# Kernel optimization log

Measured on AMD Instinct MI355X. Metric: run time of the kernel, lower is better.

The kernel has to match this reference:

```python
import jax, jax.numpy as jnp
import numpy as np

CHAR_DIM = 96
COLOR_DIM = 16
GLYPH_DIM = CHAR_DIM * COLOR_DIM  # 1536 bounded id space
CHAR_EMB = 16
COLOR_EMB = 4
GLYPH_EMB = CHAR_EMB + COLOR_EMB  # 20
HID = 32
MAX_LEN = 64


def setup_inputs() -> dict:
    key = jax.random.key(0)
    ks = jax.random.split(key, 8)
    B, H, W = 4096, 21, 79
    glyph_chars = jax.random.randint(ks[0], (B, H, W), 0, CHAR_DIM)
    glyph_colors = jax.random.randint(ks[1], (B, H, W), 0, COLOR_DIM)
    # embedding tables (row CHAR_DIM / COLOR_DIM is the padding row)
    char_table = jax.random.normal(ks[2], (CHAR_DIM + 1, CHAR_EMB), jnp.float32) * 0.1
    col_table = jax.random.normal(ks[3], (COLOR_DIM + 1, COLOR_EMB), jnp.float32) * 0.1
    s = 1.0 / np.sqrt(HID)
    Wih = jax.random.uniform(ks[4], (HID, GLYPH_EMB), jnp.float32, -s, s)
    Whh = jax.random.uniform(ks[5], (HID, HID), jnp.float32, -s, s)
    bih = jax.random.uniform(ks[6], (HID,), jnp.float32, -s, s)
    bhh = jax.random.uniform(ks[7], (HID,), jnp.float32, -s, s)
    return dict(glyph_chars=glyph_chars, glyph_colors=glyph_colors,
                char_table=char_table, col_table=col_table,
                Wih=Wih, Whh=Whh, bih=bih, bhh=bhh)


def reference(glyph_chars, glyph_colors, char_table, col_table, Wih, Whh, bih, bhh):
    B = glyph_chars.shape[0]
    # combined glyph id in the bounded [0, GLYPH_DIM) space
    ids = (glyph_chars * COLOR_DIM + glyph_colors).reshape(B, -1)  # [B, H*W]
    # batched fixed-size histogram over the bounded id space (replaces per-sample torch.unique)
    counts = jnp.zeros((B, GLYPH_DIM), jnp.int32).at[jnp.arange(B)[:, None], ids].add(1)
    present = counts > 0  # [B, GLYPH_DIM]
    # sorted unique ids (ascending == lexicographic over (char,color)); absent ids pushed to GLYPH_DIM
    sorted_ids = jnp.sort(jnp.where(present, jnp.arange(GLYPH_DIM), GLYPH_DIM), axis=-1)[:, :MAX_LEN]
    is_pad = sorted_ids >= GLYPH_DIM
    char_bag = jnp.where(is_pad, CHAR_DIM, sorted_ids // COLOR_DIM)   # pad -> CHAR_DIM row
    color_bag = jnp.where(is_pad, COLOR_DIM, sorted_ids % COLOR_DIM)  # pad -> COLOR_DIM row
    bag = jnp.stack([char_bag, color_bag], axis=-1)  # [B, MAX_LEN, 2]
    lengths = jnp.minimum(present.sum(-1), MAX_LEN)  # [B]
    emb = jnp.concatenate([char_table[char_bag], col_table[color_bag]], axis=-1)  # [B, MAX_LEN, 20]
    # vanilla tanh RNN over the packed (variable-length) bag; keep hidden at last valid step
    def step(h, inp):
        x_t, t = inp  # x_t: [B, 20]
        h_new = jnp.tanh(x_t @ Wih.T + bih + h @ Whh.T + bhh)
        h = jnp.where((t < lengths)[:, None], h_new, h)
        return h, None
    h0 = jnp.zeros((B, HID), emb.dtype)
    h, _ = jax.lax.scan(step, h0, (emb.transpose(1, 0, 2), jnp.arange(MAX_LEN)))
    return h, emb, bag
```

## Files before the change

kernel.cpp:

```cpp
#include <hip/hip_runtime.h>
#include <hip/hip_bf16.h>

#define HW        1659
#define GLYPH_DIM 1536
#define NBL       16
#define THREADS   1024

typedef _Float16 half8  __attribute__((ext_vector_type(8)));
typedef _Float16 half2v __attribute__((ext_vector_type(2)));
typedef float    f32x4  __attribute__((ext_vector_type(4)));

__device__ __forceinline__ float tanh_f(float x) {
    float e = __expf(x + x);
    return fmaf(-2.0f, __builtin_amdgcn_rcpf(e + 1.0f), 1.0f);
}

__device__ __forceinline__ unsigned int pk(float a, float b) {
    return __builtin_bit_cast(unsigned int, __builtin_amdgcn_cvt_pkrtz(a, b));
}

__device__ __forceinline__ half8 h8(unsigned int a, unsigned int b,
                                    unsigned int c, unsigned int d) {
    uint4 u = make_uint4(a, b, c, d);
    return __builtin_bit_cast(half8, u);
}

__global__ __launch_bounds__(THREADS, 4) void glyph_fused(
    const int* __restrict__ gchar, const int* __restrict__ gcol,
    const float* __restrict__ ctab, const float* __restrict__ ktab,
    const float* __restrict__ Wih, const float* __restrict__ Whh,
    const float* __restrict__ bih, const float* __restrict__ bhh,
    float* __restrict__ out_h, float* __restrict__ out_emb,
    float* __restrict__ out_bag)
{
    __shared__ unsigned int   mask[NBL][48];
    __shared__ unsigned short ids[NBL][64];
    __shared__ int            lens[NBL];
    __shared__ uint4          P_lds[64][64];

    const int tid = threadIdx.x;
    const int b0  = blockIdx.x * NBL;
    const int n   = tid & 15, g = (tid >> 4) & 3;

    half8 wihA0, wihA1;
    f32x4 bias0, bias1;
    #pragma unroll
    for (int j = 0; j < 8; ++j) {
        int k = (j < 4) ? (4 * g + j) : (12 + 4 * g + j);
        wihA0[j] = (_Float16)((k < 20) ? Wih[n * 20 + k] : 0.0f);
        wihA1[j] = (_Float16)((k < 20) ? Wih[(n + 16) * 20 + k] : 0.0f);
    }
    #pragma unroll
    for (int i = 0; i < 4; ++i) {
        bias0[i] = bih[4 * g + i] + bhh[4 * g + i];
        bias1[i] = bih[16 + 4 * g + i] + bhh[16 + 4 * g + i];
    }

    if (tid < NBL * 48) ((unsigned int*)mask)[tid] = 0u;
    __syncthreads();

    const int4* cp = (const int4*)(gchar + (long)b0 * HW);
    const int4* kp = (const int4*)(gcol  + (long)b0 * HW);
    const int n4 = (NBL * HW) / 4;
    for (int idx = tid; idx < n4; idx += THREADS) {
        int4 c = cp[idx];
        int4 k = kp[idx];
        int gg  = idx * 4;
        int bl0 = gg / HW;
        int rem = gg - bl0 * HW;
        int bl1 = bl0 + ((rem + 1) >= HW);
        int bl2 = bl0 + ((rem + 2) >= HW);
        int bl3 = bl0 + ((rem + 3) >= HW);
        int id0 = c.x * 16 + k.x;
        int id1 = c.y * 16 + k.y;
        int id2 = c.z * 16 + k.z;
        int id3 = c.w * 16 + k.w;
        atomicOr(&mask[bl0][id0 >> 5], 1u << (id0 & 31));
        atomicOr(&mask[bl1][id1 >> 5], 1u << (id1 & 31));
        atomicOr(&mask[bl2][id2 >> 5], 1u << (id2 & 31));
        atomicOr(&mask[bl3][id3 >> 5], 1u << (id3 & 31));
    }
    __syncthreads();

    if (tid < NBL * 32) {
        const int bl  = tid >> 5;
        const int l32 = tid & 31;
        unsigned long long m = 0ull;
        if (l32 < 24)
            m = ((unsigned long long)mask[bl][2 * l32 + 1] << 32) |
                (unsigned long long)mask[bl][2 * l32];
        int cnt  = __popcll(m);
        int incl = cnt;
        #pragma unroll
        for (int d = 1; d < 32; d <<= 1) {
            int nb = __shfl_up(incl, d, 32);
            if (l32 >= d) incl += nb;
        }
        int excl  = incl - cnt;
        int total = __shfl(incl, 31, 32);
        if (l32 == 0) lens[bl] = min(total, 64);
        ids[bl][l32]      = GLYPH_DIM;
        ids[bl][l32 + 32] = GLYPH_DIM;
        unsigned long long mm = m;
        int r = excl;
        while (mm != 0ull && r < 64) {
            int bit = __builtin_ctzll(mm);
            ids[bl][r] = (unsigned short)(l32 * 64 + bit);
            ++r;
            mm &= (mm - 1ull);
        }
    }
    __syncthreads();

    {
        const int nb = tid >> 6, r = tid & 63;
        int id = ids[nb][r];
        int ch = id >> 4;
        int co = (id >= GLYPH_DIM) ? 16 : (id & 15);
        const float4* crow = (const float4*)(ctab + ch * 16);
        float4 c0 = crow[0], c1 = crow[1], c2 = crow[2], c3 = crow[3];
        float4 k0 = *(const float4*)(ktab + co * 4);
        float* gp = out_emb + ((long)(b0 + nb) * 64 + r) * 20;
        *(float4*)(gp + 0)  = c0;
        *(float4*)(gp + 4)  = c1;
        *(float4*)(gp + 8)  = c2;
        *(float4*)(gp + 12) = c3;
        *(float4*)(gp + 16) = k0;
        *(float2*)(out_bag + ((long)(b0 + nb) * 64 + r) * 2) =
            make_float2((float)ch, (float)co);
    }

    {
        const int w = tid >> 6;
        #pragma unroll
        for (int i = 0; i < 4; ++i) {
            int t  = 4 * w + i;
            int id = ids[n][t];
            int ch = id >> 4;
            int co = (id >= GLYPH_DIM) ? 16 : (id & 15);
            float4 q1 = *(const float4*)(ctab + ch * 16 + 4 * g);
            float4 q2 = (g == 0) ? *(const float4*)(ktab + co * 4)
                                 : make_float4(0, 0, 0, 0);
            half8 xB = h8(pk(q1.x, q1.y), pk(q1.z, q1.w),
                          pk(q2.x, q2.y), pk(q2.z, q2.w));
            f32x4 P0 = __builtin_amdgcn_mfma_f32_16x16x32_f16(wihA0, xB, bias0, 0, 0, 0);
            f32x4 P1 = __builtin_amdgcn_mfma_f32_16x16x32_f16(wihA1, xB, bias1, 0, 0, 0);
            P_lds[t][tid & 63] = make_uint4(pk(P0[0], P0[1]), pk(P0[2], P0[3]),
                                            pk(P1[0], P1[1]), pk(P1[2], P1[3]));
        }
    }
    __syncthreads();

    if (tid < 64) {
        half8 whhA0, whhA1;
        #pragma unroll
        for (int j = 0; j < 8; ++j) {
            int k = (j < 4) ? (4 * g + j) : (12 + 4 * g + j);
            whhA0[j] = (_Float16)Whh[n * 32 + k];
            whhA1[j] = (_Float16)Whh[(n + 16) * 32 + k];
        }
        const int len = lens[n];
        uint4 pc = P_lds[0][tid];
        f32x4 d0 = {0, 0, 0, 0}, d1 = {0, 0, 0, 0};
        for (int t = 0; t < 64; ++t) {
            uint4 pn = P_lds[(t < 63) ? t + 1 : 63][tid];
            half8 pf = __builtin_bit_cast(half8, pc);
            f32x4 c0, c1;
            #pragma unroll
            for (int i = 0; i < 4; ++i) { c0[i] = (float)pf[i]; c1[i] = (float)pf[4 + i]; }
            half8 hB = h8(pk(d0[0], d0[1]), pk(d0[2], d0[3]),
                          pk(d1[0], d1[1]), pk(d1[2], d1[3]));
            f32x4 a0 = __builtin_amdgcn_mfma_f32_16x16x32_f16(whhA0, hB, c0, 0, 0, 0);
            f32x4 a1 = __builtin_amdgcn_mfma_f32_16x16x32_f16(whhA1, hB, c1, 0, 0, 0);
            bool upd = (t < len);
            #pragma unroll
            for (int i = 0; i < 4; ++i) {
                float h0 = tanh_f(a0[i]);
                float h1 = tanh_f(a1[i]);
                d0[i] = upd ? h0 : d0[i];
                d1[i] = upd ? h1 : d1[i];
            }
            pc = pn;
        }
        float* op = out_h + (long)(b0 + n) * 32;
        #pragma unroll
        for (int i = 0; i < 4; ++i) {
            op[4 * g + i]      = d0[i];
            op[16 + 4 * g + i] = d1[i];
        }
    }
}

extern "C" void kernel_launch(void* const* d_in, const int* in_sizes, int n_in,
                              void* d_out, int out_size, void* d_ws, size_t ws_size,
                              hipStream_t stream) {
    const int* gchar = (const int*)d_in[0];
    const int* gcol  = (const int*)d_in[1];
    const float* ctab = (const float*)d_in[2];
    const float* ktab = (const float*)d_in[3];
    const float* Wih  = (const float*)d_in[4];
    const float* Whh  = (const float*)d_in[5];
    const float* bih  = (const float*)d_in[6];
    const float* bhh  = (const float*)d_in[7];

    const int B = in_sizes[0] / HW;
    float* out_h   = (float*)d_out;
    float* out_emb = out_h + (long)B * 32;
    float* out_bag = out_emb + (long)B * 64 * 20;

    glyph_fused<<<B / NBL, THREADS, 0, stream>>>(
        gchar, gcol, ctab, ktab, Wih, Whh, bih, bhh, out_h, out_emb, out_bag);
}
```

Measured before the change: 39.51 us.

## Split fused kernel into histogram kernel and combined RNN/embedding kernel

Splits the single fused kernel into two. The first kernel builds the per-sample histogram and sorted ids for 4 samples per block and writes them to workspace in both batch-major and time-major layouts. The second kernel launches separate blocks for the RNN and for the embedding/bag writes. RNN blocks handle 64 samples with 4 waves, compute the input projection inline with a software pipeline, and read both tables from LDS. The aim is to remove the serialized single-wave RNN tail and raise parallelism, at the cost of a second launch and a workspace round trip.

Measured after the change: 45.78 us. 1.16x slower.

```diff
diff --git a/kernel.cpp b/kernel.cpp
--- a/kernel.cpp
+++ b/kernel.cpp
@@ -3,8 +3,6 @@
 
 #define HW        1659
 #define GLYPH_DIM 1536
-#define NBL       16
-#define THREADS   1024
 
 typedef _Float16 half8  __attribute__((ext_vector_type(8)));
 typedef _Float16 half2v __attribute__((ext_vector_type(2)));
@@ -25,64 +23,54 @@
     return __builtin_bit_cast(half8, u);
 }
 
-__global__ __launch_bounds__(THREADS, 4) void glyph_fused(
+__global__ __launch_bounds__(256, 8) void k1_histo(
     const int* __restrict__ gchar, const int* __restrict__ gcol,
-    const float* __restrict__ ctab, const float* __restrict__ ktab,
-    const float* __restrict__ Wih, const float* __restrict__ Whh,
-    const float* __restrict__ bih, const float* __restrict__ bhh,
-    float* __restrict__ out_h, float* __restrict__ out_emb,
-    float* __restrict__ out_bag)
+    unsigned short* __restrict__ ids_bt,
+    unsigned short* __restrict__ ids_tb,
+    int* __restrict__ lens_g)
 {
-    __shared__ unsigned int   mask[NBL][48];
-    __shared__ unsigned short ids[NBL][64];
-    __shared__ int            lens[NBL];
-    __shared__ uint4          P_lds[64][64];
+    __shared__ unsigned int   mask[4][48];
+    __shared__ unsigned short ids_s[4][64];
 
     const int tid = threadIdx.x;
-    const int b0  = blockIdx.x * NBL;
-    const int n   = tid & 15, g = (tid >> 4) & 3;
-
-    half8 wihA0, wihA1;
-    f32x4 bias0, bias1;
-    #pragma unroll
-    for (int j = 0; j < 8; ++j) {
-        int k = (j < 4) ? (4 * g + j) : (12 + 4 * g + j);
-        wihA0[j] = (_Float16)((k < 20) ? Wih[n * 20 + k] : 0.0f);
-        wihA1[j] = (_Float16)((k < 20) ? Wih[(n + 16) * 20 + k] : 0.0f);
-    }
-    #pragma unroll
-    for (int i = 0; i < 4; ++i) {
-        bias0[i] = bih[4 * g + i] + bhh[4 * g + i];
-        bias1[i] = bih[16 + 4 * g + i] + bhh[16 + 4 * g + i];
-    }
-
-    if (tid < NBL * 48) ((unsigned int*)mask)[tid] = 0u;
+    const int b0  = blockIdx.x * 4;
+
+    if (tid < 192) ((unsigned int*)mask)[tid] = 0u;
     __syncthreads();
 
     const int4* cp = (const int4*)(gchar + (long)b0 * HW);
     const int4* kp = (const int4*)(gcol  + (long)b0 * HW);
-    const int n4 = (NBL * HW) / 4;
-    for (int idx = tid; idx < n4; idx += THREADS) {
-        int4 c = cp[idx];
-        int4 k = kp[idx];
-        int gg  = idx * 4;
-        int bl0 = gg / HW;
-        int rem = gg - bl0 * HW;
-        int bl1 = bl0 + ((rem + 1) >= HW);
-        int bl2 = bl0 + ((rem + 2) >= HW);
-        int bl3 = bl0 + ((rem + 3) >= HW);
-        int id0 = c.x * 16 + k.x;
-        int id1 = c.y * 16 + k.y;
-        int id2 = c.z * 16 + k.z;
-        int id3 = c.w * 16 + k.w;
-        atomicOr(&mask[bl0][id0 >> 5], 1u << (id0 & 31));
-        atomicOr(&mask[bl1][id1 >> 5], 1u << (id1 & 31));
-        atomicOr(&mask[bl2][id2 >> 5], 1u << (id2 & 31));
-        atomicOr(&mask[bl3][id3 >> 5], 1u << (id3 & 31));
+    const int n4 = HW;
+    int idx = tid;
+    bool valid = idx < n4;
+    int4 c = {}, k = {};
+    if (valid) { c = cp[idx]; k = kp[idx]; }
+    while (valid) {
+        int  idx1 = idx + 256;
+        bool v1   = idx1 < n4;
+        int4 c1 = {}, k1 = {};
+        if (v1) { c1 = cp[idx1]; k1 = kp[idx1]; }
+        {
+            int gg  = idx * 4;
+            int bl0 = gg / HW;
+            int rem = gg - bl0 * HW;
+            int bl1 = bl0 + ((rem + 1) >= HW);
+            int bl2 = bl0 + ((rem + 2) >= HW);
+            int bl3 = bl0 + ((rem + 3) >= HW);
+            int id0 = c.x * 16 + k.x;
+            int id1 = c.y * 16 + k.y;
+            int id2 = c.z * 16 + k.z;
+            int id3 = c.w * 16 + k.w;
+            atomicOr(&mask[bl0][id0 >> 5], 1u << (id0 & 31));
+            atomicOr(&mask[bl1][id1 >> 5], 1u << (id1 & 31));
+            atomicOr(&mask[bl2][id2 >> 5], 1u << (id2 & 31));
+            atomicOr(&mask[bl3][id3 >> 5], 1u << (id3 & 31));
+        }
+        idx = idx1; valid = v1; c = c1; k = k1;
     }
     __syncthreads();
 
-    if (tid < NBL * 32) {
+    if (tid < 128) {
         const int bl  = tid >> 5;
         const int l32 = tid & 31;
         unsigned long long m = 0ull;
@@ -98,80 +86,102 @@
         }
         int excl  = incl - cnt;
         int total = __shfl(incl, 31, 32);
-        if (l32 == 0) lens[bl] = min(total, 64);
-        ids[bl][l32]      = GLYPH_DIM;
-        ids[bl][l32 + 32] = GLYPH_DIM;
+        if (l32 == 0) lens_g[b0 + bl] = min(total, 64);
+        ids_s[bl][l32]      = GLYPH_DIM;
+        ids_s[bl][l32 + 32] = GLYPH_DIM;
         unsigned long long mm = m;
         int r = excl;
         while (mm != 0ull && r < 64) {
             int bit = __builtin_ctzll(mm);
-            ids[bl][r] = (unsigned short)(l32 * 64 + bit);
+            ids_s[bl][r] = (unsigned short)(l32 * 64 + bit);
             ++r;
             mm &= (mm - 1ull);
         }
     }
     __syncthreads();
 
+    if (tid < 128)
+        ((unsigned int*)(ids_bt + (long)b0 * 64))[tid] = ((unsigned int*)ids_s)[tid];
     {
-        const int nb = tid >> 6, r = tid & 63;
-        int id = ids[nb][r];
-        int ch = id >> 4;
-        int co = (id >= GLYPH_DIM) ? 16 : (id & 15);
-        const float4* crow = (const float4*)(ctab + ch * 16);
-        float4 c0 = crow[0], c1 = crow[1], c2 = crow[2], c3 = crow[3];
-        float4 k0 = *(const float4*)(ktab + co * 4);
-        float* gp = out_emb + ((long)(b0 + nb) * 64 + r) * 20;
-        *(float4*)(gp + 0)  = c0;
-        *(float4*)(gp + 4)  = c1;
-        *(float4*)(gp + 8)  = c2;
-        *(float4*)(gp + 12) = c3;
-        *(float4*)(gp + 16) = k0;
-        *(float2*)(out_bag + ((long)(b0 + nb) * 64 + r) * 2) =
-            make_float2((float)ch, (float)co);
-    }
-
-    {
-        const int w = tid >> 6;
+        const int bl = tid >> 6, t = tid & 63;
+        const int b  = b0 + bl;
+        ids_tb[((long)(b >> 6) * 64 + t) * 64 + (b & 63)] = ids_s[bl][t];
+    }
+}
+
+__global__ __launch_bounds__(256, 4) void k23_main(
+    const float* __restrict__ ctab, const float* __restrict__ ktab,
+    const float* __restrict__ Wih, const float* __restrict__ Whh,
+    const float* __restrict__ bih, const float* __restrict__ bhh,
+    const unsigned short* __restrict__ ids_bt,
+    const unsigned short* __restrict__ ids_tb,
+    const int* __restrict__ lens_g,
+    float* __restrict__ out_h, float* __restrict__ out_emb,
+    float* __restrict__ out_bag, int nrnn)
+{
+    __shared__ float          tabs[1620];
+    __shared__ unsigned short ids_t[64 * 64];
+
+    const int tid = threadIdx.x;
+
+    for (int i = tid; i < 1620; i += 256)
+        tabs[i] = (i < 1552) ? ctab[i] : ktab[i - 1552];
+
+    if ((int)blockIdx.x < nrnn) {
+        {
+            const unsigned int* src = (const unsigned int*)(ids_tb + (long)blockIdx.x * 4096);
+            unsigned int* dst = (unsigned int*)ids_t;
+            #pragma unroll
+            for (int j = 0; j < 8; ++j) dst[tid + j * 256] = src[tid + j * 256];
+        }
+        const int n = tid & 15, g = (tid >> 4) & 3;
+        half8 wihA0, wihA1, whhA0, whhA1;
+        #pragma unroll
+        for (int j = 0; j < 8; ++j) {
+            int kk = (j < 4) ? (4 * g + j) : (12 + 4 * g + j);
+            wihA0[j] = (_Float16)((kk < 20) ? Wih[n * 20 + kk] : 0.0f);
+            wihA1[j] = (_Float16)((kk < 20) ? Wih[(n + 16) * 20 + kk] : 0.0f);
+            whhA0[j] = (_Float16)Whh[n * 32 + kk];
+            whhA1[j] = (_Float16)Whh[(n + 16) * 32 + kk];
+        }
+        f32x4 bias0, bias1;
         #pragma unroll
         for (int i = 0; i < 4; ++i) {
-            int t  = 4 * w + i;
-            int id = ids[n][t];
+            bias0[i] = bih[4 * g + i] + bhh[4 * g + i];
+            bias1[i] = bih[16 + 4 * g + i] + bhh[16 + 4 * g + i];
+        }
+        const int ib  = (tid >> 6) * 16 + n;
+        const int b   = blockIdx.x * 64 + ib;
+        const int len = lens_g[b];
+        __syncthreads();
+
+        auto build = [&](int id) -> half8 {
             int ch = id >> 4;
             int co = (id >= GLYPH_DIM) ? 16 : (id & 15);
-            float4 q1 = *(const float4*)(ctab + ch * 16 + 4 * g);
-            float4 q2 = (g == 0) ? *(const float4*)(ktab + co * 4)
-                                 : make_float4(0, 0, 0, 0);
-            half8 xB = h8(pk(q1.x, q1.y), pk(q1.z, q1.w),
-                          pk(q2.x, q2.y), pk(q2.z, q2.w));
-            f32x4 P0 = __builtin_amdgcn_mfma_f32_16x16x32_f16(wihA0, xB, bias0, 0, 0, 0);
-            f32x4 P1 = __builtin_amdgcn_mfma_f32_16x16x32_f16(wihA1, xB, bias1, 0, 0, 0);
-            P_lds[t][tid & 63] = make_uint4(pk(P0[0], P0[1]), pk(P0[2], P0[3]),
-                                            pk(P1[0], P1[1]), pk(P1[2], P1[3]));
-        }
-    }
-    __syncthreads();
-
-    if (tid < 64) {
-        half8 whhA0, whhA1;
-        #pragma unroll
-        for (int j = 0; j < 8; ++j) {
-            int k = (j < 4) ? (4 * g + j) : (12 + 4 * g + j);
-            whhA0[j] = (_Float16)Whh[n * 32 + k];
-            whhA1[j] = (_Float16)Whh[(n + 16) * 32 + k];
-        }
-        const int len = lens[n];
-        uint4 pc = P_lds[0][tid];
+            f32x4 q1 = *(const f32x4*)&tabs[ch * 16 + 4 * g];
+            f32x4 q2 = {0.0f, 0.0f, 0.0f, 0.0f};
+            if (g == 0) q2 = *(const f32x4*)&tabs[1552 + co * 4];
+            return h8(pk(q1[0], q1[1]), pk(q1[2], q1[3]),
+                      pk(q2[0], q2[1]), pk(q2[2], q2[3]));
+        };
+
+        half8 x0  = build(ids_t[0 * 64 + ib]);
+        f32x4 Pc0 = __builtin_amdgcn_mfma_f32_16x16x32_f16(wihA0, x0, bias0, 0, 0, 0);
+        f32x4 Pc1 = __builtin_amdgcn_mfma_f32_16x16x32_f16(wihA1, x0, bias1, 0, 0, 0);
+        int   idn = ids_t[1 * 64 + ib];
         f32x4 d0 = {0, 0, 0, 0}, d1 = {0, 0, 0, 0};
         for (int t = 0; t < 64; ++t) {
-            uint4 pn = P_lds[(t < 63) ? t + 1 : 63][tid];
-            half8 pf = __builtin_bit_cast(half8, pc);
-            f32x4 c0, c1;
-            #pragma unroll
-            for (int i = 0; i < 4; ++i) { c0[i] = (float)pf[i]; c1[i] = (float)pf[4 + i]; }
+            f32x4 Pn0 = Pc0, Pn1 = Pc1;
+            int   id2 = (t < 62) ? (int)ids_t[(t + 2) * 64 + ib] : idn;
+            if (t < 63) {
+                half8 xn = build(idn);
+                Pn0 = __builtin_amdgcn_mfma_f32_16x16x32_f16(wihA0, xn, bias0, 0, 0, 0);
+                Pn1 = __builtin_amdgcn_mfma_f32_16x16x32_f16(wihA1, xn, bias1, 0, 0, 0);
+            }
             half8 hB = h8(pk(d0[0], d0[1]), pk(d0[2], d0[3]),
                           pk(d1[0], d1[1]), pk(d1[2], d1[3]));
-            f32x4 a0 = __builtin_amdgcn_mfma_f32_16x16x32_f16(whhA0, hB, c0, 0, 0, 0);
-            f32x4 a1 = __builtin_amdgcn_mfma_f32_16x16x32_f16(whhA1, hB, c1, 0, 0, 0);
+            f32x4 a0 = __builtin_amdgcn_mfma_f32_16x16x32_f16(whhA0, hB, Pc0, 0, 0, 0);
+            f32x4 a1 = __builtin_amdgcn_mfma_f32_16x16x32_f16(whhA1, hB, Pc1, 0, 0, 0);
             bool upd = (t < len);
             #pragma unroll
             for (int i = 0; i < 4; ++i) {
@@ -180,14 +190,29 @@
                 d0[i] = upd ? h0 : d0[i];
                 d1[i] = upd ? h1 : d1[i];
             }
-            pc = pn;
-        }
-        float* op = out_h + (long)(b0 + n) * 32;
-        #pragma unroll
-        for (int i = 0; i < 4; ++i) {
-            op[4 * g + i]      = d0[i];
-            op[16 + 4 * g + i] = d1[i];
-        }
+            Pc0 = Pn0; Pc1 = Pn1; idn = id2;
+        }
+        float* op = out_h + (long)b * 32;
+        *(f32x4*)(op + 4 * g)      = d0;
+        *(f32x4*)(op + 16 + 4 * g) = d1;
+    } else {
+        __syncthreads();
+        const long row = (long)((int)blockIdx.x - nrnn) * 256 + tid;
+        int id = ids_bt[row];
+        int ch = id >> 4;
+        int co = (id >= GLYPH_DIM) ? 16 : (id & 15);
+        f32x4 c0 = *(const f32x4*)&tabs[ch * 16 + 0];
+        f32x4 c1 = *(const f32x4*)&tabs[ch * 16 + 4];
+        f32x4 c2 = *(const f32x4*)&tabs[ch * 16 + 8];
+        f32x4 c3 = *(const f32x4*)&tabs[ch * 16 + 12];
+        f32x4 k0 = *(const f32x4*)&tabs[1552 + co * 4];
+        float* gp = out_emb + row * 20;
+        *(f32x4*)(gp + 0)  = c0;
+        *(f32x4*)(gp + 4)  = c1;
+        *(f32x4*)(gp + 8)  = c2;
+        *(f32x4*)(gp + 12) = c3;
+        *(f32x4*)(gp + 16) = k0;
+        *(float2*)(out_bag + row * 2) = make_float2((float)ch, (float)co);
     }
 }
 
@@ -208,6 +233,15 @@
     float* out_emb = out_h + (long)B * 32;
     float* out_bag = out_emb + (long)B * 64 * 20;
 
-    glyph_fused<<<B / NBL, THREADS, 0, stream>>>(
-        gchar, gcol, ctab, ktab, Wih, Whh, bih, bhh, out_h, out_emb, out_bag);
-}
+    unsigned short* ids_bt = (unsigned short*)d_ws;
+    unsigned short* ids_tb = ids_bt + (long)B * 64;
+    int*            lens_g = (int*)((char*)d_ws + (long)B * 64 * 4);
+
+    k1_histo<<<B / 4, 256, 0, stream>>>(gchar, gcol, ids_bt, ids_tb, lens_g);
+
+    const int nrnn = B / 64;
+    const int nemb = (B * 64) / 256;
+    k23_main<<<nrnn + nemb, 256, 0, stream>>>(
+        ctab, ktab, Wih, Whh, bih, bhh, ids_bt, ids_tb, lens_g,
+        out_h, out_emb, out_bag, nrnn);
+}
```
